# Kernel optimization log

Hardware: AMD Instinct MI355X
Metric: run time of the kernel (lower is better)

The kernel has to match this reference:

```python
import jax, jax.numpy as jnp
import numpy as np

GAMMA = 0.01
INFER_STEP = 4


def softor(xs, axis, gamma=GAMMA):
    # gamma-scaled log-sum-exp 'soft OR', normalized if it exceeds 1 (alphaILP semantics)
    ls = gamma * jax.nn.logsumexp(xs / gamma, axis=axis)
    return ls / jnp.maximum(jnp.max(ls), 1.0)


def _clauses(x, I):
    # x: [B, G] valuations; I: [C, G, S, L] int indices into G.
    # scan over clauses to avoid materializing [C, B, G, S, L]
    def body(_, Ii):
        g = jnp.take(x, Ii, axis=1)                 # [B, G, S, L] gather
        c = softor(jnp.prod(g, axis=-1), axis=-1)   # prod over body literals, soft-OR over substitutions -> [B, G]
        return None, c
    _, Cs = jax.lax.scan(body, None, I)
    return Cs  # [C, B, G]


def _r(x, W, I):
    Cs = _clauses(x, I)                      # [C, B, G]
    Ws = jax.nn.softmax(W, axis=1)           # [m, C]
    H = jnp.einsum('mc,cbg->mbg', Ws, Cs)    # [m, B, G]
    return softor(H, axis=0)                 # [B, G]


def setup_inputs() -> dict:
    key = jax.random.key(0)
    k1, k2, k3 = jax.random.split(key, 3)
    B, G, C, S, L, m = 64, 4096, 32, 16, 4, 1
    x = jax.random.uniform(k1, (B, G), dtype=jnp.float32)       # valuation in [0,1]
    W = jax.random.uniform(k2, (m, C), dtype=jnp.float32)       # clause weights (train=True)
    I = jax.random.randint(k3, (C, G, S, L), 0, G)               # clause index tensor
    return {"x": x, "W": W, "I": I}


def reference(x, W, I):
    R = x
    for _ in range(INFER_STEP):
        # softor over stacked [prev, new] along dim 1 -> [B, 2, G] reduced over axis 1
        R = softor(jnp.stack([R, _r(R, W, I)], axis=1), axis=1)
    return R
```

## Files before the change

### kernel.cpp

```cpp
#include <hip/hip_runtime.h>
#include <hip/hip_fp16.h>

#define Bv 64
#define Gv 4096
#define Cv 32
#define Sv 16
#define NSTEP 4
#define LOG2E 1.4426950408889634f
#define LN2   0.6931471805599453f
#define GAMMA 0.01f
#define RLOG2E_G 144.26950408889634f
#define SHIFT    72.0f
#define UNSHIFT  0.4990659758388636f

#define EXP2R(x) __builtin_amdgcn_exp2f(x)
#define LOG2R(x) __builtin_amdgcn_logf(x)

struct __align__(16) h8 { __half2 h[4]; };
struct __align__(16) f8 { float4 a, b; };

__device__ __forceinline__ float wave_max(float v) {
#pragma unroll
    for (int off = 32; off > 0; off >>= 1)
        v = fmaxf(v, __shfl_xor(v, off, 64));
    return v;
}

__global__ __launch_bounds__(256) void k_itrans(const int4* __restrict__ I4,
                                                uint2* __restrict__ IT) {
    __shared__ int4 lds[64 * 17];
    int blk = blockIdx.x;
    int c = blk >> 6, gc = blk & 63;
    size_t base = ((size_t)c * Gv + gc * 64) * Sv;
#pragma unroll
    for (int i = 0; i < 4; ++i) {
        int e = threadIdx.x + i * 256;
        int4 ii = I4[base + e];
        lds[(e >> 4) * 17 + (e & 15)] = ii;
    }
    __syncthreads();
    size_t obase = (size_t)(c * 64 + gc) * 1024;
#pragma unroll
    for (int i = 0; i < 4; ++i) {
        int o = threadIdx.x + i * 256;
        int4 ii = lds[(o & 63) * 17 + (o >> 6)];
        uint2 p;
        p.x = ((unsigned)ii.x << 4) | ((unsigned)ii.y << 20);
        p.y = ((unsigned)ii.z << 4) | ((unsigned)ii.w << 20);
        IT[obase + o] = p;
    }
}

__global__ __launch_bounds__(256) void k_transpose(const float* __restrict__ x,
                                                   f8* __restrict__ Rt8,
                                                   h8* __restrict__ Rth8) {
    __shared__ float tile[64][65];
    int g0 = blockIdx.x * 64;
#pragma unroll
    for (int i = 0; i < 16; ++i) {
        int t = threadIdx.x + i * 256;
        int b = t >> 6, gi = t & 63;
        tile[gi][b] = x[b * Gv + g0 + gi];
    }
    __syncthreads();
#pragma unroll
    for (int e = 0; e < 2; ++e) {
        int idx = threadIdx.x + e * 256;
        int gi = idx & 63, oct = idx >> 6;
        float v[8];
#pragma unroll
        for (int k = 0; k < 8; ++k) v[k] = tile[gi][oct * 8 + k];
        f8 fv;
        fv.a = make_float4(v[0], v[1], v[2], v[3]);
        fv.b = make_float4(v[4], v[5], v[6], v[7]);
        Rt8[oct * Gv + g0 + gi] = fv;
        h8 hv;
#pragma unroll
        for (int j = 0; j < 4; ++j) hv.h[j] = __floats2half2_rn(v[2 * j], v[2 * j + 1]);
        Rth8[oct * Gv + g0 + gi] = hv;
    }
}

__global__ __launch_bounds__(512, 4)
void k_clauses(const h8* __restrict__ Rth8, const uint2* __restrict__ IT,
               h8* __restrict__ Csh8, float* __restrict__ Mc) {
    __shared__ h8 tbl[Gv];
    __shared__ float smax[8];
    int tid = threadIdx.x;
    int blk = blockIdx.x;
    int c    = blk >> 4;
    int oct  = (blk >> 1) & 7;
    int ghalf = blk & 1;

    const h8* __restrict__ src = Rth8 + (size_t)oct * Gv;
#pragma unroll
    for (int i = 0; i < 8; ++i) tbl[tid + i * 512] = src[tid + i * 512];
    __syncthreads();

    int lane = tid & 63, wid = tid >> 6;
    const char* tb = (const char*)tbl;
    float vmax = 0.0f;

#pragma unroll
    for (int iter = 0; iter < 4; ++iter) {
        int gc = ghalf * 32 + wid * 4 + iter;
        const uint2* __restrict__ Ig = IT + (size_t)(c * 64 + gc) * 1024 + lane;

        float sum[8];
#pragma unroll
        for (int e = 0; e < 8; ++e) sum[e] = 0.0f;

#pragma unroll
        for (int s = 0; s < Sv; ++s) {
            uint2 u = Ig[s * 64];
            unsigned a0 = u.x & 0xFFFFu, a1 = u.x >> 16;
            unsigned a2 = u.y & 0xFFFFu, a3 = u.y >> 16;
            h8 A = *(const h8*)(tb + a0);
            h8 B = *(const h8*)(tb + a1);
            h8 E = *(const h8*)(tb + a2);
            h8 D = *(const h8*)(tb + a3);
#pragma unroll
            for (int j = 0; j < 4; ++j) {
                __half2 q = __hmul2(__hmul2(A.h[j], B.h[j]), __hmul2(E.h[j], D.h[j]));
                sum[2 * j]     += EXP2R(fmaf(__low2float(q),  RLOG2E_G, -SHIFT));
                sum[2 * j + 1] += EXP2R(fmaf(__high2float(q), RLOG2E_G, -SHIFT));
            }
        }

        float ls[8];
#pragma unroll
        for (int e = 0; e < 8; ++e)
            ls[e] = fmaf(GAMMA * LN2, LOG2R(sum[e]), UNSHIFT);

        h8 outv;
#pragma unroll
        for (int j = 0; j < 4; ++j)
            outv.h[j] = __floats2half2_rn(ls[2 * j], ls[2 * j + 1]);
        Csh8[((size_t)c * 8 + oct) * Gv + gc * 64 + lane] = outv;

#pragma unroll
        for (int e = 0; e < 8; ++e) vmax = fmaxf(vmax, ls[e]);
    }

    vmax = wave_max(vmax);
    if (lane == 0) smax[wid] = vmax;
    __syncthreads();
    if (tid == 0) {
        float m = smax[0];
#pragma unroll
        for (int i = 1; i < 8; ++i) m = fmaxf(m, smax[i]);
        atomicMax((int*)(Mc + c), __float_as_int(m));
    }
}

__global__ __launch_bounds__(256) void k_combupd(const h8* __restrict__ Csh8,
                                                 const float* __restrict__ W,
                                                 const float* __restrict__ Mc,
                                                 const f8* __restrict__ Rt8,
                                                 f8* __restrict__ Lraw8,
                                                 float* __restrict__ Lmax) {
    __shared__ float smax[4];
    __shared__ float scoef[Cv];
    if (threadIdx.x < Cv) {
        int c = threadIdx.x;
        float e = EXP2R(W[c] * LOG2E);
        float wsum = e;
#pragma unroll
        for (int off = 16; off > 0; off >>= 1)
            wsum += __shfl_xor(wsum, off, 64);
        scoef[c] = e / (wsum * fmaxf(Mc[c], 1.0f));
    }
    __syncthreads();

    int tid = blockIdx.x * 256 + threadIdx.x;
    float h[8];
#pragma unroll
    for (int e = 0; e < 8; ++e) h[e] = 0.0f;
#pragma unroll
    for (int c = 0; c < Cv; ++c) {
        float w = scoef[c];
        h8 v = Csh8[(size_t)c * (Gv * 8) + tid];
#pragma unroll
        for (int j = 0; j < 4; ++j) {
            h[2 * j]     = fmaf(w, __low2float(v.h[j]),  h[2 * j]);
            h[2 * j + 1] = fmaf(w, __high2float(v.h[j]), h[2 * j + 1]);
        }
    }

    f8 r = Rt8[tid];
    const float* rp = &r.a.x;
    f8 outv;
    float* op = &outv.a.x;
    float vmax = 0.0f;
#pragma unroll
    for (int e = 0; e < 8; ++e) {
        float hn = h[e];
        float rv = rp[e];
        float mx = fmaxf(rv, hn), mn = fminf(rv, hn);
        float t  = EXP2R((mn - mx) * RLOG2E_G);
        float ls = fmaf(GAMMA * LN2, LOG2R(1.0f + t), mx);
        op[e] = ls;
        vmax = fmaxf(vmax, ls);
    }
    Lraw8[tid] = outv;
    {
        vmax = wave_max(vmax);
        int lane = threadIdx.x & 63, wid = threadIdx.x >> 6;
        if (lane == 0) smax[wid] = vmax;
        __syncthreads();
        if (threadIdx.x == 0) {
            float m = fmaxf(fmaxf(smax[0], smax[1]), fmaxf(smax[2], smax[3]));
            atomicMax((int*)Lmax, __float_as_int(m));
        }
    }
}

__global__ __launch_bounds__(256) void k_norm(const float4* __restrict__ Lraw4,
                                              const float* __restrict__ Lmax,
                                              float4* __restrict__ Rt4,
                                              __half2* __restrict__ Rth2,
                                              float* __restrict__ out,
                                              int last) {
    int tid = blockIdx.x * 256 + threadIdx.x;
    float d = fmaxf(Lmax[0], 1.0f);
    float4 lv = Lraw4[tid];
    float4 v;
    v.x = lv.x / d; v.y = lv.y / d; v.z = lv.z / d; v.w = lv.w / d;
    if (last) {
        int lin = tid * 4;
        int oct = lin >> 15;
        int g   = (lin >> 3) & (Gv - 1);
        int k0  = lin & 7;
        int b   = oct * 8 + k0;
        out[(b + 0) * Gv + g] = v.x;
        out[(b + 1) * Gv + g] = v.y;
        out[(b + 2) * Gv + g] = v.z;
        out[(b + 3) * Gv + g] = v.w;
    } else {
        Rt4[tid] = v;
        Rth2[2 * tid]     = __floats2half2_rn(v.x, v.y);
        Rth2[2 * tid + 1] = __floats2half2_rn(v.z, v.w);
    }
}

extern "C" void kernel_launch(void* const* d_in, const int* in_sizes, int n_in,
                              void* d_out, int out_size, void* d_ws, size_t ws_size,
                              hipStream_t stream) {
    const float* x = (const float*)d_in[0];
    const float* W = (const float*)d_in[1];
    const int*   I = (const int*)d_in[2];
    float* out = (float*)d_out;

    float*  ws   = (float*)d_ws;
    float*  Rt   = ws;
    float*  Lraw = ws + 262144;
    float*  maxb = ws + 524288;
    __half* Rth  = (__half*)(ws + 524544);
    __half* Csh  = (__half*)(ws + 1048576);
    uint2*  ITp  = (uint2*) (ws + 5242880);

    (void)hipMemsetAsync(maxb, 0, NSTEP * 64 * sizeof(float), stream);
    k_itrans   <<<Cv * 64, 256, 0, stream>>>((const int4*)I, ITp);
    k_transpose<<<Gv / 64, 256, 0, stream>>>(x, (f8*)Rt, (h8*)Rth);

    for (int step = 0; step < NSTEP; ++step) {
        float* Mc = maxb + step * 64;
        float* Lm = Mc + 33;
        k_clauses<<<512, 512, 0, stream>>>((const h8*)Rth, (const uint2*)ITp,
                                           (h8*)Csh, Mc);
        k_combupd<<<(Bv * Gv) / 2048, 256, 0, stream>>>((const h8*)Csh, W, Mc,
                                                        (const f8*)Rt, (f8*)Lraw, Lm);
        k_norm   <<<(Bv * Gv) / 1024, 256, 0, stream>>>((const float4*)Lraw, Lm,
                                                        (float4*)Rt, (__half2*)Rth,
                                                        out, step == NSTEP - 1);
    }
}
```

Measured before the change: 180.7 us.

## Fold normalization into consumer kernels and drop per-step norm pass

Removes the separate per-step normalization kernel. Unnormalized log-sum-exp outputs are now ping-ponged between two buffers, and the previous step's max is applied as a reciprocal scale when k_clauses builds its fp16 LDS table and when k_combupd reads the previous valuation. A final k_out kernel normalizes and transposes only once at the end. This saves three launches and the full read/write passes over the B×G state per step. In exchange, k_clauses reads fp32 instead of fp16 (twice the load bytes into LDS) and divides by a reciprocal multiply, which can shift rounding slightly.

```diff
diff --git a/kernel.cpp b/kernel.cpp
--- a/kernel.cpp
+++ b/kernel.cpp
@@ -52,8 +52,7 @@
 }
 
 __global__ __launch_bounds__(256) void k_transpose(const float* __restrict__ x,
-                                                   f8* __restrict__ Rt8,
-                                                   h8* __restrict__ Rth8) {
+                                                   f8* __restrict__ L8) {
     __shared__ float tile[64][65];
     int g0 = blockIdx.x * 64;
 #pragma unroll
@@ -67,23 +66,19 @@
     for (int e = 0; e < 2; ++e) {
         int idx = threadIdx.x + e * 256;
         int gi = idx & 63, oct = idx >> 6;
-        float v[8];
-#pragma unroll
-        for (int k = 0; k < 8; ++k) v[k] = tile[gi][oct * 8 + k];
         f8 fv;
-        fv.a = make_float4(v[0], v[1], v[2], v[3]);
-        fv.b = make_float4(v[4], v[5], v[6], v[7]);
-        Rt8[oct * Gv + g0 + gi] = fv;
-        h8 hv;
-#pragma unroll
-        for (int j = 0; j < 4; ++j) hv.h[j] = __floats2half2_rn(v[2 * j], v[2 * j + 1]);
-        Rth8[oct * Gv + g0 + gi] = hv;
+        fv.a = make_float4(tile[gi][oct * 8 + 0], tile[gi][oct * 8 + 1],
+                           tile[gi][oct * 8 + 2], tile[gi][oct * 8 + 3]);
+        fv.b = make_float4(tile[gi][oct * 8 + 4], tile[gi][oct * 8 + 5],
+                           tile[gi][oct * 8 + 6], tile[gi][oct * 8 + 7]);
+        L8[oct * Gv + g0 + gi] = fv;
     }
 }
 
 __global__ __launch_bounds__(512, 4)
-void k_clauses(const h8* __restrict__ Rth8, const uint2* __restrict__ IT,
-               h8* __restrict__ Csh8, float* __restrict__ Mc) {
+void k_clauses(const f8* __restrict__ Lprev, const float* __restrict__ LmPrev,
+               const uint2* __restrict__ IT, h8* __restrict__ Csh8,
+               float* __restrict__ Mc) {
     __shared__ h8 tbl[Gv];
     __shared__ float smax[8];
     int tid = threadIdx.x;
@@ -92,9 +87,18 @@
     int oct  = (blk >> 1) & 7;
     int ghalf = blk & 1;
 
-    const h8* __restrict__ src = Rth8 + (size_t)oct * Gv;
-#pragma unroll
-    for (int i = 0; i < 8; ++i) tbl[tid + i * 512] = src[tid + i * 512];
+    float rd = 1.0f / fmaxf(LmPrev[0], 1.0f);
+    const f8* __restrict__ src = Lprev + (size_t)oct * Gv;
+#pragma unroll
+    for (int i = 0; i < 8; ++i) {
+        f8 v = src[tid + i * 512];
+        h8 hv;
+        hv.h[0] = __floats2half2_rn(v.a.x * rd, v.a.y * rd);
+        hv.h[1] = __floats2half2_rn(v.a.z * rd, v.a.w * rd);
+        hv.h[2] = __floats2half2_rn(v.b.x * rd, v.b.y * rd);
+        hv.h[3] = __floats2half2_rn(v.b.z * rd, v.b.w * rd);
+        tbl[tid + i * 512] = hv;
+    }
     __syncthreads();
 
     int lane = tid & 63, wid = tid >> 6;
@@ -156,9 +160,10 @@
 __global__ __launch_bounds__(256) void k_combupd(const h8* __restrict__ Csh8,
                                                  const float* __restrict__ W,
                                                  const float* __restrict__ Mc,
-                                                 const f8* __restrict__ Rt8,
-                                                 f8* __restrict__ Lraw8,
-                                                 float* __restrict__ Lmax) {
+                                                 const f8* __restrict__ Lprev,
+                                                 const float* __restrict__ LmPrev,
+                                                 f8* __restrict__ Lout,
+                                                 float* __restrict__ LmOut) {
     __shared__ float smax[4];
     __shared__ float scoef[Cv];
     if (threadIdx.x < Cv) {
@@ -187,7 +192,8 @@
         }
     }
 
-    f8 r = Rt8[tid];
+    float rd = 1.0f / fmaxf(LmPrev[0], 1.0f);
+    f8 r = Lprev[tid];
     const float* rp = &r.a.x;
     f8 outv;
     float* op = &outv.a.x;
@@ -195,52 +201,39 @@
 #pragma unroll
     for (int e = 0; e < 8; ++e) {
         float hn = h[e];
-        float rv = rp[e];
+        float rv = rp[e] * rd;
         float mx = fmaxf(rv, hn), mn = fminf(rv, hn);
         float t  = EXP2R((mn - mx) * RLOG2E_G);
         float ls = fmaf(GAMMA * LN2, LOG2R(1.0f + t), mx);
         op[e] = ls;
         vmax = fmaxf(vmax, ls);
     }
-    Lraw8[tid] = outv;
-    {
-        vmax = wave_max(vmax);
-        int lane = threadIdx.x & 63, wid = threadIdx.x >> 6;
-        if (lane == 0) smax[wid] = vmax;
-        __syncthreads();
-        if (threadIdx.x == 0) {
-            float m = fmaxf(fmaxf(smax[0], smax[1]), fmaxf(smax[2], smax[3]));
-            atomicMax((int*)Lmax, __float_as_int(m));
-        }
-    }
-}
-
-__global__ __launch_bounds__(256) void k_norm(const float4* __restrict__ Lraw4,
-                                              const float* __restrict__ Lmax,
-                                              float4* __restrict__ Rt4,
-                                              __half2* __restrict__ Rth2,
-                                              float* __restrict__ out,
-                                              int last) {
+    Lout[tid] = outv;
+    vmax = wave_max(vmax);
+    int lane = threadIdx.x & 63, wid = threadIdx.x >> 6;
+    if (lane == 0) smax[wid] = vmax;
+    __syncthreads();
+    if (threadIdx.x == 0) {
+        float m = fmaxf(fmaxf(smax[0], smax[1]), fmaxf(smax[2], smax[3]));
+        atomicMax((int*)LmOut, __float_as_int(m));
+    }
+}
+
+__global__ __launch_bounds__(256) void k_out(const float4* __restrict__ Lraw4,
+                                             const float* __restrict__ Lm,
+                                             float* __restrict__ out) {
     int tid = blockIdx.x * 256 + threadIdx.x;
-    float d = fmaxf(Lmax[0], 1.0f);
+    float d = fmaxf(Lm[0], 1.0f);
     float4 lv = Lraw4[tid];
-    float4 v;
-    v.x = lv.x / d; v.y = lv.y / d; v.z = lv.z / d; v.w = lv.w / d;
-    if (last) {
-        int lin = tid * 4;
-        int oct = lin >> 15;
-        int g   = (lin >> 3) & (Gv - 1);
-        int k0  = lin & 7;
-        int b   = oct * 8 + k0;
-        out[(b + 0) * Gv + g] = v.x;
-        out[(b + 1) * Gv + g] = v.y;
-        out[(b + 2) * Gv + g] = v.z;
-        out[(b + 3) * Gv + g] = v.w;
-    } else {
-        Rt4[tid] = v;
-        Rth2[2 * tid]     = __floats2half2_rn(v.x, v.y);
-        Rth2[2 * tid + 1] = __floats2half2_rn(v.z, v.w);
-    }
+    int lin = tid * 4;
+    int oct = lin >> 15;
+    int g   = (lin >> 3) & (Gv - 1);
+    int k0  = lin & 7;
+    int b   = oct * 8 + k0;
+    out[(b + 0) * Gv + g] = lv.x / d;
+    out[(b + 1) * Gv + g] = lv.y / d;
+    out[(b + 2) * Gv + g] = lv.z / d;
+    out[(b + 3) * Gv + g] = lv.w / d;
 }
 
 extern "C" void kernel_launch(void* const* d_in, const int* in_sizes, int n_in,
@@ -251,27 +244,29 @@
     const int*   I = (const int*)d_in[2];
     float* out = (float*)d_out;
 
-    float*  ws   = (float*)d_ws;
-    float*  Rt   = ws;
-    float*  Lraw = ws + 262144;
-    float*  maxb = ws + 524288;
-    __half* Rth  = (__half*)(ws + 524544);
-    __half* Csh  = (__half*)(ws + 1048576);
-    uint2*  ITp  = (uint2*) (ws + 5242880);
-
-    (void)hipMemsetAsync(maxb, 0, NSTEP * 64 * sizeof(float), stream);
+    float*  ws    = (float*)d_ws;
+    f8*     LrawA = (f8*)ws;
+    f8*     LrawB = (f8*)(ws + 262144);
+    float*  maxb  = ws + 524288;
+    __half* Csh   = (__half*)(ws + 1048576);
+    uint2*  ITp   = (uint2*) (ws + 5242880);
+
+    (void)hipMemsetAsync(maxb, 0, (NSTEP * 64 + 64) * sizeof(float), stream);
     k_itrans   <<<Cv * 64, 256, 0, stream>>>((const int4*)I, ITp);
-    k_transpose<<<Gv / 64, 256, 0, stream>>>(x, (f8*)Rt, (h8*)Rth);
-
+    k_transpose<<<Gv / 64, 256, 0, stream>>>(x, LrawA);
+
+    const float* LmPrev = maxb + NSTEP * 64;
+    f8* prev = LrawA;
+    f8* cur  = LrawB;
     for (int step = 0; step < NSTEP; ++step) {
         float* Mc = maxb + step * 64;
-        float* Lm = Mc + 33;
-        k_clauses<<<512, 512, 0, stream>>>((const h8*)Rth, (const uint2*)ITp,
+        float* Lm = Mc + 32;
+        k_clauses<<<512, 512, 0, stream>>>(prev, LmPrev, (const uint2*)ITp,
                                            (h8*)Csh, Mc);
         k_combupd<<<(Bv * Gv) / 2048, 256, 0, stream>>>((const h8*)Csh, W, Mc,
-                                                        (const f8*)Rt, (f8*)Lraw, Lm);
-        k_norm   <<<(Bv * Gv) / 1024, 256, 0, stream>>>((const float4*)Lraw, Lm,
-                                                        (float4*)Rt, (__half2*)Rth,
-                                                        out, step == NSTEP - 1);
-    }
-}
+                                                        prev, LmPrev, cur, Lm);
+        LmPrev = Lm;
+        f8* t = prev; prev = cur; cur = t;
+    }
+    k_out<<<(Bv * Gv) / 1024, 256, 0, stream>>>((const float4*)prev, LmPrev, out);
+}
```

Measured after the change: 175.2 us. 3.1% less time.
